# Kernel optimization log

Hardware: AMD Instinct MI355X
Metric: run time of the kernel (lower is better)

Reference implementation:

```python
import jax, jax.numpy as jnp
import numpy as np


def _conv1x1(x, W, b):
    # 1x1 conv == per-pixel channel matmul: x [B,C,H,W], W [O,C], b [O]
    return jnp.einsum('bchw,oc->bohw', x, W) + b[None, :, None, None]


def setup_inputs() -> dict:
    key = jax.random.key(0)
    ks = jax.random.split(key, 9)
    B, C, H, W = 16, 512, 32, 32
    s = 1.0 / np.sqrt(C)
    inp = {
        'x': jax.random.normal(ks[0], (B, C, H, W), dtype=jnp.float32),
        'Wq': jax.random.normal(ks[1], (C, C), dtype=jnp.float32) * s,
        'bq': jax.random.normal(ks[2], (C,), dtype=jnp.float32) * 0.01,
        'Wk': jax.random.normal(ks[3], (C, C), dtype=jnp.float32) * s,
        'bk': jax.random.normal(ks[4], (C,), dtype=jnp.float32) * 0.01,
        'Wv': jax.random.normal(ks[5], (C, C), dtype=jnp.float32) * s,
        'bv': jax.random.normal(ks[6], (C,), dtype=jnp.float32) * 0.01,
        'Wo': jax.random.normal(ks[7], (C, C), dtype=jnp.float32) * s,
        'bo': jax.random.normal(ks[8], (C,), dtype=jnp.float32) * 0.01,
    }
    return inp


def reference(x, Wq, bq, Wk, bk, Wv, bv, Wo, bo):
    B, C, H, W = x.shape
    q = _conv1x1(x, Wq, bq)
    k = _conv1x1(x, Wk, bk)
    v = _conv1x1(x, Wv, bv)
    hw = H * W
    qf = q.reshape(B, C, hw)  # [B,C,HW]
    kf = k.reshape(B, C, hw)
    vf = v.reshape(B, C, hw)
    # scores[b,i,j] = sum_c q[b,c,i] * k[b,c,j], scaled by c^-0.5
    scores = jnp.einsum('bci,bcj->bij', qf, kf) * (C ** -0.5)
    attn = jax.nn.softmax(scores, axis=2)  # softmax over keys j
    # out[b,c,i] = sum_j v[b,c,j] * attn[b,i,j]
    out = jnp.einsum('bcj,bij->bci', vf, attn).reshape(B, C, H, W)
    out = _conv1x1(out, Wo, bo)
    return x + out
```

## Files before the change

kernel.cpp:

```cpp
#include <hip/hip_runtime.h>
#include <hip/hip_bf16.h>
#include <math.h>


typedef __bf16 bf16x8 __attribute__((ext_vector_type(8)));
typedef float  f32x4  __attribute__((ext_vector_type(4)));

__device__ __forceinline__ unsigned short f2bf(float f) {
    unsigned u = __float_as_uint(f);
    u += 0x7fff + ((u >> 16) & 1);
    return (unsigned short)(u >> 16);
}

__device__ __forceinline__ void gload_lds16(const void* g, void* l) {
    __builtin_amdgcn_global_load_lds(
        (const __attribute__((address_space(1))) void*)g,
        (__attribute__((address_space(3))) void*)l, 16, 0, 0);
}

struct GemmP {
    const unsigned short* A;
    const unsigned short* B;
    void* C;
    const float* bias;
    const float* resid;
    int M, N, K, ldA, ldB;
    long sA, sB, sC, sR;
    int ln_nn, ln_pb;
    float scale;
};

template<bool OUT_F32, int BIAS_MODE, bool RESID, int EXPM>
__device__ __forceinline__ void gemm_body(const GemmP p, int L,
                                          unsigned short* Als,
                                          unsigned short* Bls)
{
    const int xcd = L & 7;
    const int idx = L >> 3;
    const int bz  = xcd * 2 + (idx >> p.ln_pb);
    const int w   = idx & ((1 << p.ln_pb) - 1);
    const int m0  = (w >> p.ln_nn) << 8;
    const int n0  = (w & ((1 << p.ln_nn) - 1)) << 7;

    const unsigned short* A = p.A + bz * p.sA;
    const unsigned short* B = p.B + bz * p.sB;

    const int tid  = threadIdx.x;
    const int lane = tid & 63;
    const int wave = tid >> 6;
    const int wr   = wave >> 1;
    const int wc   = wave & 1;

    const int ar = lane >> 2;
    const int ak = ((lane & 3) ^ ((ar >> 1) & 3)) * 8;

    const unsigned short* agp = A + (long)(m0 + wave * 16 + ar) * p.ldA + ak;
    const unsigned short* bgp = B + (long)(n0 + wave * 16 + ar) * p.ldB + ak;
    const long aj = 128L * p.ldA;

    const int fr = lane & 15;
    const int fq = lane >> 4;
    const int kphys = (fq ^ ((fr >> 1) & 3)) * 8;

    f32x4 acc[4][4] = {};
    f32x4 acc1[4] = {};
    bf16x8 ones;
    if constexpr (EXPM == 2) {
        #pragma unroll
        for (int i = 0; i < 8; ++i) ones[i] = (__bf16)1.0f;
    }

    const int nsteps = p.K >> 5;

    auto STAGE = [&](int sel) {
        unsigned short* a0 = Als + sel * 8192;
        unsigned short* b0 = Bls + sel * 4096;
        gload_lds16(agp,      a0 + wave * 512);
        gload_lds16(agp + aj, a0 + (wave + 8) * 512);
        gload_lds16(bgp,      b0 + wave * 512);
        agp += 32; bgp += 32;
    };

    auto COMPUTE = [&](int sel) {
        const unsigned short* Ap = Als + sel * 8192;
        const unsigned short* Bp = Bls + sel * 4096;
        bf16x8 af[4], bfr[4];
        #pragma unroll
        for (int mt = 0; mt < 4; ++mt)
            af[mt] = *(const bf16x8*)&Ap[(wr * 64 + mt * 16 + fr) * 32 + kphys];
        #pragma unroll
        for (int nt = 0; nt < 4; ++nt)
            bfr[nt] = *(const bf16x8*)&Bp[(wc * 64 + nt * 16 + fr) * 32 + kphys];
        __builtin_amdgcn_s_setprio(1);
        if constexpr (EXPM == 2) {
            #pragma unroll
            for (int mt = 0; mt < 4; ++mt)
                acc1[mt] = __builtin_amdgcn_mfma_f32_16x16x32_bf16(
                    af[mt], ones, acc1[mt], 0, 0, 0);
        }
        #pragma unroll
        for (int mt = 0; mt < 4; ++mt)
            #pragma unroll
            for (int nt = 0; nt < 4; ++nt)
                acc[mt][nt] = __builtin_amdgcn_mfma_f32_16x16x32_bf16(
                    af[mt], bfr[nt], acc[mt][nt], 0, 0, 0);
        __builtin_amdgcn_s_setprio(0);
    };

    STAGE(0);
    STAGE(1);

    int bc = 0, bn = 1, bs = 2;
    for (int t = 0; t < nsteps - 1; ++t) {
        __builtin_amdgcn_sched_barrier(0);
        asm volatile("s_waitcnt vmcnt(3)" ::: "memory");
        __builtin_amdgcn_s_barrier();
        asm volatile("" ::: "memory");
        __builtin_amdgcn_sched_barrier(0);
        if (t + 2 < nsteps) STAGE(bs);
        COMPUTE(bc);
        const int tmp = bc; bc = bn; bn = bs; bs = tmp;
    }
    __builtin_amdgcn_sched_barrier(0);
    asm volatile("s_waitcnt vmcnt(0)" ::: "memory");
    __builtin_amdgcn_s_barrier();
    asm volatile("" ::: "memory");
    __builtin_amdgcn_sched_barrier(0);
    COMPUTE(bc);

    float* Cf = (float*)p.C + bz * p.sC;
    unsigned short* Ch = (unsigned short*)p.C + bz * p.sC;
    const float* resid = RESID ? (p.resid + bz * p.sR) : nullptr;
    const int N = p.N;

    if constexpr (EXPM == 1) {
        #pragma unroll
        for (int mt = 0; mt < 4; ++mt)
            #pragma unroll
            for (int r = 0; r < 4; ++r) {
                const int row = m0 + wr * 64 + mt * 16 + fq * 4 + r;
                #pragma unroll
                for (int nt = 0; nt < 4; ++nt) {
                    const int col = n0 + wc * 64 + nt * 16 + fr;
                    Ch[(long)row * N + col] = f2bf(__expf(acc[mt][nt][r] * p.scale));
                }
            }
    } else {
        #pragma unroll
        for (int mt = 0; mt < 4; ++mt) {
            float linv[4];
            if constexpr (EXPM == 2) {
                #pragma unroll
                for (int r = 0; r < 4; ++r)
                    linv[r] = 1.0f / acc1[mt][r];
            }
            #pragma unroll
            for (int nt = 0; nt < 4; ++nt) {
                const int col = n0 + wc * 64 + nt * 16 + fr;
                const float bn2 = (BIAS_MODE == 2) ? p.bias[col] : 0.0f;
                #pragma unroll
                for (int r = 0; r < 4; ++r) {
                    const int row = m0 + wr * 64 + mt * 16 + fq * 4 + r;
                    float val = acc[mt][nt][r] + bn2;
                    if (BIAS_MODE == 1) val += p.bias[row];
                    if constexpr (EXPM == 2) val *= linv[r];
                    const long o = (long)row * N + col;
                    if (RESID) val += resid[o];
                    if (OUT_F32) Cf[o] = val;
                    else         Ch[o] = f2bf(val);
                }
            }
        }
    }
}

template<bool OUT_F32, int BIAS_MODE, bool RESID, int EXPM>
__global__ __launch_bounds__(512, 4) void gemm_bt_mfma(GemmP p)
{
    __shared__ unsigned short Als[3 * 8192];
    __shared__ unsigned short Bls[3 * 4096];
    gemm_body<OUT_F32, BIAS_MODE, RESID, EXPM>(p, blockIdx.x, Als, Bls);
}

__global__ __launch_bounds__(512, 4) void gemm_qkv_fused(GemmP pqk, GemmP pv, int split)
{
    __shared__ unsigned short Als[3 * 8192];
    __shared__ unsigned short Bls[3 * 4096];
    if ((int)blockIdx.x < split)
        gemm_body<false, 2, false, 0>(pqk, blockIdx.x, Als, Bls);
    else
        gemm_body<false, 1, false, 0>(pv, blockIdx.x - split, Als, Bls);
}

__global__ __launch_bounds__(256) void prep_all(
    const float* __restrict__ x, unsigned short* __restrict__ xT,
    const float* __restrict__ Wq, const float* __restrict__ Wk,
    const float* __restrict__ Wv, const float* __restrict__ Wo,
    const float* __restrict__ bq, const float* __restrict__ bk,
    unsigned short* __restrict__ Wb, float* __restrict__ biasqk)
{
    const int b = blockIdx.x;
    const int t = threadIdx.x;
    if (b < 2048) {
        __shared__ unsigned short tlb[64 * 64];
        const int batch = b >> 7;
        const int rem = b & 127;
        const int c0 = (rem >> 4) * 64;
        const int p0 = (rem & 15) * 64;
        const float* xb = x + (long)batch * 524288;
        unsigned short* xTb = xT + (long)batch * 524288;
        const int lx = t & 15;
        const int ly = t >> 4;
        #pragma unroll
        for (int i = 0; i < 4; ++i) {
            const int c = ly + 16 * i;
            const float4 f = *(const float4*)&xb[(long)(c0 + c) * 1024 + p0 + lx * 4];
            ushort4 h;
            h.x = f2bf(f.x); h.y = f2bf(f.y); h.z = f2bf(f.z); h.w = f2bf(f.w);
            const int colp = (lx * 4) ^ (((c >> 3) & 7) << 3);
            *(ushort4*)&tlb[c * 64 + colp] = h;
        }
        __syncthreads();
        const int sx = t & 7;
        const int sy = t >> 3;
        #pragma unroll
        for (int i = 0; i < 2; ++i) {
            const int r = sy + 32 * i;
            ushort4 lo, hi;
            lo.x = tlb[(sx * 8 + 0) * 64 + (r ^ (sx << 3))];
            lo.y = tlb[(sx * 8 + 1) * 64 + (r ^ (sx << 3))];
            lo.z = tlb[(sx * 8 + 2) * 64 + (r ^ (sx << 3))];
            lo.w = tlb[(sx * 8 + 3) * 64 + (r ^ (sx << 3))];
            hi.x = tlb[(sx * 8 + 4) * 64 + (r ^ (sx << 3))];
            hi.y = tlb[(sx * 8 + 5) * 64 + (r ^ (sx << 3))];
            hi.z = tlb[(sx * 8 + 6) * 64 + (r ^ (sx << 3))];
            hi.w = tlb[(sx * 8 + 7) * 64 + (r ^ (sx << 3))];
            unsigned short* o = &xTb[(long)(p0 + r) * 512 + c0 + sx * 8];
            *(ushort4*)o = lo;
            *(ushort4*)(o + 4) = hi;
        }
    } else if (b < 3072) {
        const int wb = b - 2048;
        const float* srcs[4] = {Wq, Wk, Wv, Wo};
        const float* s = srcs[wb >> 8];
        unsigned short* d = Wb + (long)(wb >> 8) * 262144;
        const int i = ((wb & 255) * 256 + t) * 4;
        const float4 f = *(const float4*)(s + i);
        ushort4 h;
        h.x = f2bf(f.x); h.y = f2bf(f.y); h.z = f2bf(f.z); h.w = f2bf(f.w);
        *(ushort4*)(d + i) = h;
    } else {
        biasqk[t]       = bq[t];
        biasqk[256 + t] = bq[256 + t];
        biasqk[512 + t] = bk[t];
        biasqk[768 + t] = bk[256 + t];
    }
}

extern "C" void kernel_launch(void* const* d_in, const int* in_sizes, int n_in,
                              void* d_out, int out_size, void* d_ws, size_t ws_size,
                              hipStream_t stream)
{
    const float* x  = (const float*)d_in[0];
    const float* Wq = (const float*)d_in[1];
    const float* bq = (const float*)d_in[2];
    const float* Wk = (const float*)d_in[3];
    const float* bk = (const float*)d_in[4];
    const float* Wv = (const float*)d_in[5];
    const float* bv = (const float*)d_in[6];
    const float* Wo = (const float*)d_in[7];
    const float* bo = (const float*)d_in[8];
    float* out = (float*)d_out;

    const int Bn = 16, C = 512, HW = 1024;
    const long CHW = (long)C * HW;
    const long SHW = (long)HW * HW;

    unsigned short* xT   = (unsigned short*)d_ws;
    unsigned short* qkT  = xT + Bn * CHW;
    unsigned short* vB   = qkT + Bn * SHW;
    unsigned short* expS = vB + Bn * CHW;
    unsigned short* Wb   = expS + Bn * SHW;
    float* biasqk = (float*)(Wb + 4 * 262144);
    unsigned short* OT = xT;

    unsigned short* Wvb = Wb + 2 * 262144;
    unsigned short* Wob = Wb + 3 * 262144;

    const dim3 blk(512);
    const float scale = 0.044194173824159216f;

    prep_all<<<dim3(3073), dim3(256), 0, stream>>>(x, xT, Wq, Wk, Wv, Wo,
                                                   bq, bk, Wb, biasqk);

    GemmP pqk = { xT, Wb, qkT, biasqk, nullptr,
                  HW, 2 * C, C, C, C, CHW, 0, SHW, 0, 3, 5, 0.0f };
    GemmP pv  = { Wvb, xT, vB, bv, nullptr,
                  C, HW, C, C, C, 0, CHW, CHW, 0, 3, 4, 0.0f };
    gemm_qkv_fused<<<dim3(768), blk, 0, stream>>>(pqk, pv, 512);

    GemmP ps  = { qkT, qkT + C, expS, nullptr, nullptr,
                  HW, HW, C, 2 * C, 2 * C, SHW, SHW, SHW, 0, 3, 5, scale };
    gemm_bt_mfma<false, 0, false, 1><<<dim3(512), blk, 0, stream>>>(ps);

    GemmP po  = { expS, vB, OT, nullptr, nullptr,
                  HW, C, HW, HW, HW, SHW, CHW, CHW, 0, 2, 4, 0.0f };
    gemm_bt_mfma<false, 0, false, 2><<<dim3(256), blk, 0, stream>>>(po);

    GemmP pout = { Wob, OT, out, bo, x,
                   C, HW, C, C, C, 0, CHW, CHW, CHW, 3, 4, 0.0f };
    gemm_bt_mfma<true, 1, true, 0><<<dim3(256), blk, 0, stream>>>(pout);
}
```

Measured before the change: 217.7 us.

## Templatize GEMM tile shape, enlarge tiles and deepen LDS pipeline to four stages

Makes the MFMA GEMM body generic over per-wave tile counts (MT, NT), giving block tiles of 256x256, 256x128 or 128x256 depending on the stage. The wave layout changes to 2x4. The LDS ring grows from three to four buffers with three loads in flight, and the launch grids shrink to 256 or 512 blocks. Larger tiles increase data reuse per LDS load and the deeper prefetch hides more global latency. In exchange, register and LDS use rise, occupancy bound drops to 2 blocks per CU, and fewer blocks may leave CUs underfilled.

```diff
diff --git a/kernel.cpp b/kernel.cpp
--- a/kernel.cpp
+++ b/kernel.cpp
@@ -16,6 +16,14 @@
     __builtin_amdgcn_global_load_lds(
         (const __attribute__((address_space(1))) void*)g,
         (__attribute__((address_space(3))) void*)l, 16, 0, 0);
+}
+
+template<int N> __device__ __forceinline__ void waitcnt_vm() {
+    if constexpr (N == 0) asm volatile("s_waitcnt vmcnt(0)" ::: "memory");
+    else if constexpr (N == 3) asm volatile("s_waitcnt vmcnt(3)" ::: "memory");
+    else if constexpr (N == 4) asm volatile("s_waitcnt vmcnt(4)" ::: "memory");
+    else if constexpr (N == 6) asm volatile("s_waitcnt vmcnt(6)" ::: "memory");
+    else if constexpr (N == 8) asm volatile("s_waitcnt vmcnt(8)" ::: "memory");
 }
 
 struct GemmP {
@@ -26,21 +34,28 @@
     const float* resid;
     int M, N, K, ldA, ldB;
     long sA, sB, sC, sR;
-    int ln_nn, ln_pb;
     float scale;
 };
 
-template<bool OUT_F32, int BIAS_MODE, bool RESID, int EXPM>
+template<int MT, int NT, bool OUT_F32, int BIAS_MODE, bool RESID, int EXPM>
 __device__ __forceinline__ void gemm_body(const GemmP p, int L,
                                           unsigned short* Als,
                                           unsigned short* Bls)
 {
+    constexpr int BM   = MT * 32;
+    constexpr int BN   = NT * 64;
+    constexpr int APAN = BM * 32;
+    constexpr int BPAN = BN * 32;
+    constexpr int ACH  = BM / 128;
+    constexpr int BCH  = BN / 128;
+    constexpr int LPS  = ACH + BCH;
+
     const int xcd = L & 7;
     const int idx = L >> 3;
-    const int bz  = xcd * 2 + (idx >> p.ln_pb);
-    const int w   = idx & ((1 << p.ln_pb) - 1);
-    const int m0  = (w >> p.ln_nn) << 8;
-    const int n0  = (w & ((1 << p.ln_nn) - 1)) << 7;
+    const int bz  = xcd * 2 + (idx >> 4);
+    const int w   = idx & 15;
+    const int m0  = (w >> 2) * BM;
+    const int n0  = (w & 3) * BN;
 
     const unsigned short* A = p.A + bz * p.sA;
     const unsigned short* B = p.B + bz * p.sB;
@@ -48,8 +63,8 @@
     const int tid  = threadIdx.x;
     const int lane = tid & 63;
     const int wave = tid >> 6;
-    const int wr   = wave >> 1;
-    const int wc   = wave & 1;
+    const int wm   = wave >> 2;
+    const int wn   = wave & 3;
 
     const int ar = lane >> 2;
     const int ak = ((lane & 3) ^ ((ar >> 1) & 3)) * 8;
@@ -57,13 +72,14 @@
     const unsigned short* agp = A + (long)(m0 + wave * 16 + ar) * p.ldA + ak;
     const unsigned short* bgp = B + (long)(n0 + wave * 16 + ar) * p.ldB + ak;
     const long aj = 128L * p.ldA;
+    const long bj = 128L * p.ldB;
 
     const int fr = lane & 15;
     const int fq = lane >> 4;
-    const int kphys = (fq ^ ((fr >> 1) & 3)) * 8;
-
-    f32x4 acc[4][4] = {};
-    f32x4 acc1[4] = {};
+    const int kph = (fq ^ ((fr >> 1) & 3)) * 8;
+
+    f32x4 acc[MT][NT] = {};
+    f32x4 acc1[MT] = {};
     bf16x8 ones;
     if constexpr (EXPM == 2) {
         #pragma unroll
@@ -73,60 +89,64 @@
     const int nsteps = p.K >> 5;
 
     auto STAGE = [&](int sel) {
-        unsigned short* a0 = Als + sel * 8192;
-        unsigned short* b0 = Bls + sel * 4096;
-        gload_lds16(agp,      a0 + wave * 512);
-        gload_lds16(agp + aj, a0 + (wave + 8) * 512);
-        gload_lds16(bgp,      b0 + wave * 512);
+        unsigned short* a0 = Als + sel * APAN;
+        unsigned short* b0 = Bls + sel * BPAN;
+        gload_lds16(agp, a0 + wave * 512);
+        if constexpr (ACH == 2) gload_lds16(agp + aj, a0 + (wave + 8) * 512);
+        gload_lds16(bgp, b0 + wave * 512);
+        if constexpr (BCH == 2) gload_lds16(bgp + bj, b0 + (wave + 8) * 512);
         agp += 32; bgp += 32;
     };
 
     auto COMPUTE = [&](int sel) {
-        const unsigned short* Ap = Als + sel * 8192;
-        const unsigned short* Bp = Bls + sel * 4096;
-        bf16x8 af[4], bfr[4];
-        #pragma unroll
-        for (int mt = 0; mt < 4; ++mt)
-            af[mt] = *(const bf16x8*)&Ap[(wr * 64 + mt * 16 + fr) * 32 + kphys];
-        #pragma unroll
-        for (int nt = 0; nt < 4; ++nt)
-            bfr[nt] = *(const bf16x8*)&Bp[(wc * 64 + nt * 16 + fr) * 32 + kphys];
+        const unsigned short* Ap = Als + sel * APAN;
+        const unsigned short* Bp = Bls + sel * BPAN;
+        bf16x8 af[MT], bfr[NT];
+        #pragma unroll
+        for (int mt = 0; mt < MT; ++mt)
+            af[mt] = *(const bf16x8*)&Ap[(wm * MT * 16 + mt * 16 + fr) * 32 + kph];
+        #pragma unroll
+        for (int nt = 0; nt < NT; ++nt)
+            bfr[nt] = *(const bf16x8*)&Bp[(wn * NT * 16 + nt * 16 + fr) * 32 + kph];
         __builtin_amdgcn_s_setprio(1);
         if constexpr (EXPM == 2) {
             #pragma unroll
-            for (int mt = 0; mt < 4; ++mt)
+            for (int mt = 0; mt < MT; ++mt)
                 acc1[mt] = __builtin_amdgcn_mfma_f32_16x16x32_bf16(
                     af[mt], ones, acc1[mt], 0, 0, 0);
         }
         #pragma unroll
-        for (int mt = 0; mt < 4; ++mt)
+        for (int mt = 0; mt < MT; ++mt)
             #pragma unroll
-            for (int nt = 0; nt < 4; ++nt)
+            for (int nt = 0; nt < NT; ++nt)
                 acc[mt][nt] = __builtin_amdgcn_mfma_f32_16x16x32_bf16(
                     af[mt], bfr[nt], acc[mt][nt], 0, 0, 0);
         __builtin_amdgcn_s_setprio(0);
     };
 
-    STAGE(0);
-    STAGE(1);
-
-    int bc = 0, bn = 1, bs = 2;
-    for (int t = 0; t < nsteps - 1; ++t) {
+    STAGE(0); STAGE(1); STAGE(2);
+
+    for (int t = 0; t < nsteps - 2; ++t) {
         __builtin_amdgcn_sched_barrier(0);
-        asm volatile("s_waitcnt vmcnt(3)" ::: "memory");
+        waitcnt_vm<2 * LPS>();
         __builtin_amdgcn_s_barrier();
         asm volatile("" ::: "memory");
         __builtin_amdgcn_sched_barrier(0);
-        if (t + 2 < nsteps) STAGE(bs);
-        COMPUTE(bc);
-        const int tmp = bc; bc = bn; bn = bs; bs = tmp;
+        if (t + 3 < nsteps) STAGE((t + 3) & 3);
+        COMPUTE(t & 3);
     }
     __builtin_amdgcn_sched_barrier(0);
-    asm volatile("s_waitcnt vmcnt(0)" ::: "memory");
+    waitcnt_vm<LPS>();
     __builtin_amdgcn_s_barrier();
     asm volatile("" ::: "memory");
     __builtin_amdgcn_sched_barrier(0);
-    COMPUTE(bc);
+    COMPUTE((nsteps - 2) & 3);
+    __builtin_amdgcn_sched_barrier(0);
+    waitcnt_vm<0>();
+    __builtin_amdgcn_s_barrier();
+    asm volatile("" ::: "memory");
+    __builtin_amdgcn_sched_barrier(0);
+    COMPUTE((nsteps - 1) & 3);
 
     float* Cf = (float*)p.C + bz * p.sC;
     unsigned short* Ch = (unsigned short*)p.C + bz * p.sC;
@@ -135,19 +155,19 @@
 
     if constexpr (EXPM == 1) {
         #pragma unroll
-        for (int mt = 0; mt < 4; ++mt)
+        for (int mt = 0; mt < MT; ++mt)
             #pragma unroll
             for (int r = 0; r < 4; ++r) {
-                const int row = m0 + wr * 64 + mt * 16 + fq * 4 + r;
+                const int row = m0 + wm * MT * 16 + mt * 16 + fq * 4 + r;
                 #pragma unroll
-                for (int nt = 0; nt < 4; ++nt) {
-                    const int col = n0 + wc * 64 + nt * 16 + fr;
+                for (int nt = 0; nt < NT; ++nt) {
+                    const int col = n0 + wn * NT * 16 + nt * 16 + fr;
                     Ch[(long)row * N + col] = f2bf(__expf(acc[mt][nt][r] * p.scale));
                 }
             }
     } else {
         #pragma unroll
-        for (int mt = 0; mt < 4; ++mt) {
+        for (int mt = 0; mt < MT; ++mt) {
             float linv[4];
             if constexpr (EXPM == 2) {
                 #pragma unroll
@@ -155,12 +175,12 @@
                     linv[r] = 1.0f / acc1[mt][r];
             }
             #pragma unroll
-            for (int nt = 0; nt < 4; ++nt) {
-                const int col = n0 + wc * 64 + nt * 16 + fr;
+            for (int nt = 0; nt < NT; ++nt) {
+                const int col = n0 + wn * NT * 16 + nt * 16 + fr;
                 const float bn2 = (BIAS_MODE == 2) ? p.bias[col] : 0.0f;
                 #pragma unroll
                 for (int r = 0; r < 4; ++r) {
-                    const int row = m0 + wr * 64 + mt * 16 + fq * 4 + r;
+                    const int row = m0 + wm * MT * 16 + mt * 16 + fq * 4 + r;
                     float val = acc[mt][nt][r] + bn2;
                     if (BIAS_MODE == 1) val += p.bias[row];
                     if constexpr (EXPM == 2) val *= linv[r];
@@ -174,22 +194,23 @@
     }
 }
 
-template<bool OUT_F32, int BIAS_MODE, bool RESID, int EXPM>
-__global__ __launch_bounds__(512, 4) void gemm_bt_mfma(GemmP p)
-{
-    __shared__ unsigned short Als[3 * 8192];
-    __shared__ unsigned short Bls[3 * 4096];
-    gemm_body<OUT_F32, BIAS_MODE, RESID, EXPM>(p, blockIdx.x, Als, Bls);
-}
-
-__global__ __launch_bounds__(512, 4) void gemm_qkv_fused(GemmP pqk, GemmP pv, int split)
-{
-    __shared__ unsigned short Als[3 * 8192];
-    __shared__ unsigned short Bls[3 * 4096];
-    if ((int)blockIdx.x < split)
-        gemm_body<false, 2, false, 0>(pqk, blockIdx.x, Als, Bls);
+template<int MT, int NT, bool OUT_F32, int BIAS_MODE, bool RESID, int EXPM>
+__global__ __launch_bounds__(512, 2) void gemm_k(GemmP p)
+{
+    __shared__ unsigned short Als[4 * MT * 1024];
+    __shared__ unsigned short Bls[4 * NT * 2048];
+    gemm_body<MT, NT, OUT_F32, BIAS_MODE, RESID, EXPM>(p, blockIdx.x, Als, Bls);
+}
+
+__global__ __launch_bounds__(512, 2) void gemm_qkv_fused(GemmP pqk, GemmP pv)
+{
+    __shared__ unsigned short LDS[65536];
+    if ((int)blockIdx.x < 256)
+        gemm_body<8, 4, false, 2, false, 0>(pqk, blockIdx.x,
+                                            LDS, LDS + 4 * 8 * 1024);
     else
-        gemm_body<false, 1, false, 0>(pv, blockIdx.x - split, Als, Bls);
+        gemm_body<4, 4, false, 1, false, 0>(pv, blockIdx.x - 256,
+                                            LDS, LDS + 4 * 4 * 1024);
 }
 
 __global__ __launch_bounds__(256) void prep_all(
@@ -272,7 +293,8 @@
     const float* bo = (const float*)d_in[8];
     float* out = (float*)d_out;
 
-    const int Bn = 16, C = 512, HW = 1024;
+    const int C = 512, HW = 1024;
+    const int Bn = 16;
     const long CHW = (long)C * HW;
     const long SHW = (long)HW * HW;
 
@@ -287,27 +309,26 @@
     unsigned short* Wvb = Wb + 2 * 262144;
     unsigned short* Wob = Wb + 3 * 262144;
 
-    const dim3 blk(512);
     const float scale = 0.044194173824159216f;
 
     prep_all<<<dim3(3073), dim3(256), 0, stream>>>(x, xT, Wq, Wk, Wv, Wo,
                                                    bq, bk, Wb, biasqk);
 
     GemmP pqk = { xT, Wb, qkT, biasqk, nullptr,
-                  HW, 2 * C, C, C, C, CHW, 0, SHW, 0, 3, 5, 0.0f };
+                  HW, 2 * C, C, C, C, CHW, 0, SHW, 0, 0.0f };
     GemmP pv  = { Wvb, xT, vB, bv, nullptr,
-                  C, HW, C, C, C, 0, CHW, CHW, 0, 3, 4, 0.0f };
-    gemm_qkv_fused<<<dim3(768), blk, 0, stream>>>(pqk, pv, 512);
+                  C, HW, C, C, C, 0, CHW, CHW, 0, 0.0f };
+    gemm_qkv_fused<<<dim3(512), dim3(512), 0, stream>>>(pqk, pv);
 
     GemmP ps  = { qkT, qkT + C, expS, nullptr, nullptr,
-                  HW, HW, C, 2 * C, 2 * C, SHW, SHW, SHW, 0, 3, 5, scale };
-    gemm_bt_mfma<false, 0, false, 1><<<dim3(512), blk, 0, stream>>>(ps);
+                  HW, HW, C, 2 * C, 2 * C, SHW, SHW, SHW, 0, scale };
+    gemm_k<8, 4, false, 0, false, 1><<<dim3(256), dim3(512), 0, stream>>>(ps);
 
     GemmP po  = { expS, vB, OT, nullptr, nullptr,
-                  HW, C, HW, HW, HW, SHW, CHW, CHW, 0, 2, 4, 0.0f };
-    gemm_bt_mfma<false, 0, false, 2><<<dim3(256), blk, 0, stream>>>(po);
+                  HW, C, HW, HW, HW, SHW, CHW, CHW, 0, 0.0f };
+    gemm_k<8, 2, false, 0, false, 2><<<dim3(256), dim3(512), 0, stream>>>(po);
 
     GemmP pout = { Wob, OT, out, bo, x,
-                   C, HW, C, C, C, 0, CHW, CHW, CHW, 3, 4, 0.0f };
-    gemm_bt_mfma<true, 1, true, 0><<<dim3(256), blk, 0, stream>>>(pout);
-}
+                   C, HW, C, C, C, 0, CHW, CHW, CHW, 0.0f };
+    gemm_k<4, 4, true, 1, true, 0><<<dim3(256), dim3(512), 0, stream>>>(pout);
+}
```

Measured after the change: 219.4 us. Within noise of the previous version (+0.8%).
